# Optimization experiments

Measured on AMD Instinct MI355X. Metric: run time of the kernel, lower is better.

The kernel has to match this reference:

```python
import jax, jax.numpy as jnp
import numpy as np

N_NODES = 50000
IN_DIM = 256
LATENT = 128
HIDDEN = 2 * LATENT  # 256


def _xavier(key, fan_in, fan_out):
    # matches nn.init.xavier_uniform_ on a [out, in] weight; we store as [in, out]
    limit = float(np.sqrt(6.0 / (fan_in + fan_out)))
    return jax.random.uniform(key, (fan_in, fan_out), jnp.float32, -limit, limit)


def setup_inputs() -> dict:
    key = jax.random.key(0)
    ks = jax.random.split(key, 8)
    x = jax.random.normal(ks[0], (N_NODES, IN_DIM), jnp.float32)
    edge_index = jax.random.randint(ks[1], (2, 800000), 0, N_NODES, jnp.int64)
    W1 = _xavier(ks[2], IN_DIM, HIDDEN)
    b1 = jnp.zeros((HIDDEN,), jnp.float32)
    Wmu = _xavier(ks[3], HIDDEN, LATENT)
    bmu = jnp.zeros((LATENT,), jnp.float32)
    Wlv = _xavier(ks[4], HIDDEN, LATENT)
    blv = jnp.zeros((LATENT,), jnp.float32)
    return {"x": x, "edge_index": edge_index, "W1": W1, "b1": b1,
            "Wmu": Wmu, "bmu": bmu, "Wlv": Wlv, "blv": blv}


def _gcn_layer(x, W, b, src, dst):
    # PyG GCNConv: h = x @ W; add self loops; symmetric norm; scatter-add; + bias
    h = x @ W  # [N, out]
    ones = jnp.ones(src.shape[0], x.dtype)
    deg = jax.ops.segment_sum(ones, dst, num_segments=N_NODES) + 1.0  # +1 for self loop
    dinv = jax.lax.rsqrt(deg)  # deg >= 1 always
    norm = dinv[src] * dinv[dst]  # [E]
    agg = jax.ops.segment_sum(h[src] * norm[:, None], dst, num_segments=N_NODES)
    agg = agg + h * (dinv * dinv)[:, None]  # self-loop contribution, norm_ii = 1/deg_i
    return agg + b


def reference(x, edge_index, W1, b1, Wmu, bmu, Wlv, blv):
    src, dst = edge_index[0], edge_index[1]
    z = _gcn_layer(x, W1, b1, src, dst)
    z = jax.nn.relu(z)
    # dropout in eval mode == identity
    mu = _gcn_layer(z, Wmu, bmu, src, dst)
    logvar = _gcn_layer(z, Wlv, blv, src, dst)
    return (mu, logvar)
```

## Files before the change

kernel.cpp:

```cpp
#include <hip/hip_runtime.h>

#define N_NODES 50000
#define E_EDGES 800000
#define D 256
#define L 128
#define CAP 64

typedef __attribute__((ext_vector_type(8))) short bf16x8;
typedef __attribute__((ext_vector_type(4))) float f32x4;

__device__ __forceinline__ float bf2f(unsigned short u) {
    union { unsigned int i; float f; } v; v.i = ((unsigned int)u) << 16; return v.f;
}
__device__ __forceinline__ unsigned short f2bf(float f) {
    union { float f; unsigned int i; } v; v.f = f;
    unsigned int r = v.i + 0x7fffu + ((v.i >> 16) & 1u);
    return (unsigned short)(r >> 16);
}

__global__ __launch_bounds__(256) void setup_t(
    const float* __restrict__ W1, const float* __restrict__ Wmu,
    const float* __restrict__ Wlv, const float* __restrict__ bmu,
    const float* __restrict__ blv,
    unsigned short* __restrict__ W1h, unsigned short* __restrict__ W1l,
    unsigned short* __restrict__ Wch,
    float* __restrict__ bcat, int* __restrict__ cursor) {
    int b = blockIdx.x, t = threadIdx.x;
    if (b < 128) {
        __shared__ float tile[32][33];
        int m = b >> 6;
        int ti = b & 63;
        int k0 = (ti >> 3) * 32, n0 = (ti & 7) * 32;
        int rr = t >> 5, cc = t & 31;
#pragma unroll
        for (int p = 0; p < 4; ++p) {
            int kk = p * 8 + rr;
            int k = k0 + kk, n = n0 + cc;
            float w;
            if (m == 0) w = W1[k * 256 + n];
            else        w = (n < 128) ? Wmu[k * 128 + n] : Wlv[k * 128 + (n - 128)];
            tile[kk][cc] = w;
        }
        __syncthreads();
#pragma unroll
        for (int p = 0; p < 4; ++p) {
            int nn = p * 8 + rr;
            float w = tile[cc][nn];
            unsigned short h = f2bf(w);
            int n = n0 + nn, k = k0 + cc;
            if (m == 0) {
                W1h[n * 256 + k] = h;
                W1l[n * 256 + k] = f2bf(w - bf2f(h));
            } else {
                Wch[n * 256 + k] = h;
            }
        }
        if (b == 64) bcat[t] = (t < 128) ? bmu[t] : blv[t - 128];
    } else {
        int i = (b - 128) * 256 + t;
        if (i < N_NODES) cursor[i] = 0;
    }
}

__global__ __launch_bounds__(256, 2) void gemm1_fill(
    const float* __restrict__ A,
    const unsigned short* __restrict__ Bth, const unsigned short* __restrict__ Btl,
    unsigned short* __restrict__ Hout, int M,
    const int* __restrict__ src, const int* __restrict__ dst,
    int* __restrict__ cursor, unsigned short* __restrict__ bucket)
{
    __shared__ unsigned short Ash[128 * 32];
    __shared__ unsigned short Asl[128 * 32];
    __shared__ unsigned short Bsh[256 * 32];
    __shared__ unsigned short Bsl[256 * 32];
    const int bid = blockIdx.x;
    const int qb = bid / 9, rb = bid - qb * 9;
    const int t = threadIdx.x;

    if (rb != 0) {
        int e = (bid - qb - 1) * 256 + t;
        if (e < E_EDGES) {
            int d = dst[e];
            int pos = atomicAdd(&cursor[d], 1);
            if (pos < CAP) bucket[d * CAP + pos] = (unsigned short)src[e];
        }
        return;
    }

    const int lane = t & 63, wave = t >> 6;
    const int m_ = lane & 15, q = lane >> 4;
    const int wr = wave >> 1, wc = wave & 1;
    const int row0 = qb * 128;
    const int sr = t >> 2;
    const int sc = t & 3;

    f32x4 acc[4][8];
    const f32x4 zf = {0.f, 0.f, 0.f, 0.f};
#pragma unroll
    for (int rs = 0; rs < 4; ++rs)
#pragma unroll
        for (int nt = 0; nt < 8; ++nt) acc[rs][nt] = zf;

    for (int ks = 0; ks < 8; ++ks) {
        const int k0 = ks * 32;
        bf16x8 gbh[4], gbl[4];
#pragma unroll
        for (int i = 0; i < 4; ++i) {
            int n = sr + i * 64;
            gbh[i] = *(const bf16x8*)(Bth + n * 256 + k0 + sc * 8);
            gbl[i] = *(const bf16x8*)(Btl + n * 256 + k0 + sc * 8);
        }
        float4 ga0[2], ga1[2];
#pragma unroll
        for (int p = 0; p < 2; ++p) {
            int r = row0 + p * 64 + sr; if (r >= M) r = M - 1;
            const float* Xp = A + (size_t)r * 256 + k0 + sc * 8;
            ga0[p] = *(const float4*)Xp;
            ga1[p] = *(const float4*)(Xp + 4);
        }
        __syncthreads();
#pragma unroll
        for (int p = 0; p < 2; ++p) {
            int lr = p * 64 + sr;
            int cc = (sc ^ ((lr >> 1) & 3)) * 8;
            float af[8] = {ga0[p].x, ga0[p].y, ga0[p].z, ga0[p].w,
                           ga1[p].x, ga1[p].y, ga1[p].z, ga1[p].w};
            bf16x8 h, l;
#pragma unroll
            for (int j = 0; j < 8; ++j) {
                unsigned short hh = f2bf(af[j]);
                h[j] = (short)hh;
                l[j] = (short)f2bf(af[j] - bf2f(hh));
            }
            *(bf16x8*)&Ash[lr * 32 + cc] = h;
            *(bf16x8*)&Asl[lr * 32 + cc] = l;
        }
#pragma unroll
        for (int i = 0; i < 4; ++i) {
            int n = sr + i * 64;
            int cc = (sc ^ ((n >> 1) & 3)) * 8;
            *(bf16x8*)&Bsh[n * 32 + cc] = gbh[i];
            *(bf16x8*)&Bsl[n * 32 + cc] = gbl[i];
        }
        __syncthreads();
        bf16x8 ah[4], al[4];
#pragma unroll
        for (int rs = 0; rs < 4; ++rs) {
            int r = wr * 64 + rs * 16 + m_;
            int cc = (q ^ ((r >> 1) & 3)) * 8;
            ah[rs] = *(const bf16x8*)&Ash[r * 32 + cc];
            al[rs] = *(const bf16x8*)&Asl[r * 32 + cc];
        }
#pragma unroll
        for (int nt = 0; nt < 8; ++nt) {
            int n = wc * 128 + nt * 16 + m_;
            int cr = (q ^ ((n >> 1) & 3)) * 8;
            bf16x8 bh = *(const bf16x8*)&Bsh[n * 32 + cr];
            bf16x8 bl = *(const bf16x8*)&Bsl[n * 32 + cr];
#pragma unroll
            for (int rs = 0; rs < 4; ++rs) {
                acc[rs][nt] = __builtin_amdgcn_mfma_f32_16x16x32_bf16(ah[rs], bh, acc[rs][nt], 0, 0, 0);
                acc[rs][nt] = __builtin_amdgcn_mfma_f32_16x16x32_bf16(ah[rs], bl, acc[rs][nt], 0, 0, 0);
                acc[rs][nt] = __builtin_amdgcn_mfma_f32_16x16x32_bf16(al[rs], bh, acc[rs][nt], 0, 0, 0);
            }
        }
    }
#pragma unroll
    for (int rs = 0; rs < 4; ++rs) {
        int rbase = row0 + wr * 64 + rs * 16 + q * 4;
#pragma unroll
        for (int rr = 0; rr < 4; ++rr) {
            int grow = rbase + rr;
            if (grow >= M) continue;
#pragma unroll
            for (int nt = 0; nt < 8; ++nt) {
                int gcol = wc * 128 + nt * 16 + m_;
                Hout[(size_t)grow * 256 + gcol] = f2bf(acc[rs][nt][rr]);
            }
        }
    }
}

__global__ __launch_bounds__(256, 2) void gemm_bf16(
    const unsigned short* __restrict__ A,
    const unsigned short* __restrict__ Bth,
    unsigned short* __restrict__ Tout, int M)
{
    __shared__ unsigned short Ash[128 * 32];
    __shared__ unsigned short Bsh[256 * 32];
    const int t = threadIdx.x;
    const int lane = t & 63, wave = t >> 6;
    const int m_ = lane & 15, q = lane >> 4;
    const int wr = wave >> 1, wc = wave & 1;
    const int row0 = blockIdx.x * 128;
    const int sr = t >> 2;
    const int sc = t & 3;

    f32x4 acc[4][8];
    const f32x4 zf = {0.f, 0.f, 0.f, 0.f};
#pragma unroll
    for (int rs = 0; rs < 4; ++rs)
#pragma unroll
        for (int nt = 0; nt < 8; ++nt) acc[rs][nt] = zf;

    for (int ks = 0; ks < 8; ++ks) {
        const int k0 = ks * 32;
        bf16x8 gbh[4];
#pragma unroll
        for (int i = 0; i < 4; ++i) {
            int n = sr + i * 64;
            gbh[i] = *(const bf16x8*)(Bth + n * 256 + k0 + sc * 8);
        }
        bf16x8 gav[2];
#pragma unroll
        for (int p = 0; p < 2; ++p) {
            int r = row0 + p * 64 + sr; if (r >= M) r = M - 1;
            gav[p] = *(const bf16x8*)(A + (size_t)r * 256 + k0 + sc * 8);
        }
        __syncthreads();
#pragma unroll
        for (int p = 0; p < 2; ++p) {
            int lr = p * 64 + sr;
            int cc = (sc ^ ((lr >> 1) & 3)) * 8;
            *(bf16x8*)&Ash[lr * 32 + cc] = gav[p];
        }
#pragma unroll
        for (int i = 0; i < 4; ++i) {
            int n = sr + i * 64;
            int cc = (sc ^ ((n >> 1) & 3)) * 8;
            *(bf16x8*)&Bsh[n * 32 + cc] = gbh[i];
        }
        __syncthreads();
        bf16x8 ah[4];
#pragma unroll
        for (int rs = 0; rs < 4; ++rs) {
            int r = wr * 64 + rs * 16 + m_;
            int cc = (q ^ ((r >> 1) & 3)) * 8;
            ah[rs] = *(const bf16x8*)&Ash[r * 32 + cc];
        }
#pragma unroll
        for (int nt = 0; nt < 8; ++nt) {
            int n = wc * 128 + nt * 16 + m_;
            int cr = (q ^ ((n >> 1) & 3)) * 8;
            bf16x8 bh = *(const bf16x8*)&Bsh[n * 32 + cr];
#pragma unroll
            for (int rs = 0; rs < 4; ++rs) {
                acc[rs][nt] = __builtin_amdgcn_mfma_f32_16x16x32_bf16(ah[rs], bh, acc[rs][nt], 0, 0, 0);
            }
        }
    }
#pragma unroll
    for (int rs = 0; rs < 4; ++rs) {
        int rbase = row0 + wr * 64 + rs * 16 + q * 4;
#pragma unroll
        for (int rr = 0; rr < 4; ++rr) {
            int grow = rbase + rr;
            if (grow >= M) continue;
#pragma unroll
            for (int nt = 0; nt < 8; ++nt) {
                int gcol = wc * 128 + nt * 16 + m_;
                Tout[(size_t)grow * 256 + gcol] = f2bf(acc[rs][nt][rr]);
            }
        }
    }
}

__global__ __launch_bounds__(256) void gather_pre(
    const unsigned short* __restrict__ Hs,
    const unsigned short* __restrict__ bucket, const int* __restrict__ cnt_,
    const float* __restrict__ bias,
    unsigned short* __restrict__ OutZ,
    float* __restrict__ mu, float* __restrict__ lv, int mode, int node0)
{
    const int lane = threadIdx.x & 63;
    const int hl = lane & 31;
    const int bb = lane & 32;
    const int node = node0 + blockIdx.x * 8 + (threadIdx.x >> 5);
    const int col = hl * 8;
    int raw = cnt_[node];
    float dn = rsqrtf((float)raw + 1.0f);
    int cnt = raw > CAP ? CAP : raw;

    int   s0r = 0, s1r = 0;
    float w0r = 0.f, w1r = 0.f;
    if (hl < cnt) {
        s0r = (int)bucket[node * CAP + hl];
        w0r = rsqrtf((float)cnt_[s0r] + 1.0f) * dn;
    }
    if (hl + 32 < cnt) {
        s1r = (int)bucket[node * CAP + 32 + hl];
        w1r = rsqrtf((float)cnt_[s1r] + 1.0f) * dn;
    }

    float sl = dn * dn;
    bf16x8 hv = *(const bf16x8*)(Hs + (size_t)node * D + col);
    float a[8];
#pragma unroll
    for (int p = 0; p < 8; ++p) a[p] = bf2f((unsigned short)hv[p]) * sl;

    const int cnt0 = cnt < 32 ? cnt : 32;
    int j = 0;
    for (; j + 3 < cnt0; j += 4) {
        int t0 = __shfl(s0r, bb + j,     64), t1 = __shfl(s0r, bb + j + 1, 64);
        int t2 = __shfl(s0r, bb + j + 2, 64), t3 = __shfl(s0r, bb + j + 3, 64);
        float w0 = __shfl(w0r, bb + j,     64), w1 = __shfl(w0r, bb + j + 1, 64);
        float w2 = __shfl(w0r, bb + j + 2, 64), w3 = __shfl(w0r, bb + j + 3, 64);
        bf16x8 u0 = *(const bf16x8*)(Hs + (size_t)t0 * D + col);
        bf16x8 u1 = *(const bf16x8*)(Hs + (size_t)t1 * D + col);
        bf16x8 u2 = *(const bf16x8*)(Hs + (size_t)t2 * D + col);
        bf16x8 u3 = *(const bf16x8*)(Hs + (size_t)t3 * D + col);
#pragma unroll
        for (int p = 0; p < 8; ++p) a[p] = fmaf(bf2f((unsigned short)u0[p]), w0, a[p]);
#pragma unroll
        for (int p = 0; p < 8; ++p) a[p] = fmaf(bf2f((unsigned short)u1[p]), w1, a[p]);
#pragma unroll
        for (int p = 0; p < 8; ++p) a[p] = fmaf(bf2f((unsigned short)u2[p]), w2, a[p]);
#pragma unroll
        for (int p = 0; p < 8; ++p) a[p] = fmaf(bf2f((unsigned short)u3[p]), w3, a[p]);
    }
    for (; j < cnt0; ++j) {
        int   t0 = __shfl(s0r, bb + j, 64);
        float w0 = __shfl(w0r, bb + j, 64);
        bf16x8 u0 = *(const bf16x8*)(Hs + (size_t)t0 * D + col);
#pragma unroll
        for (int p = 0; p < 8; ++p) a[p] = fmaf(bf2f((unsigned short)u0[p]), w0, a[p]);
    }
    if (cnt > 32) {
        for (int j2 = 0; j2 < cnt - 32; ++j2) {
            int   t0 = __shfl(s1r, bb + j2, 64);
            float w0 = __shfl(w1r, bb + j2, 64);
            bf16x8 u0 = *(const bf16x8*)(Hs + (size_t)t0 * D + col);
#pragma unroll
            for (int p = 0; p < 8; ++p) a[p] = fmaf(bf2f((unsigned short)u0[p]), w0, a[p]);
        }
    }

    float4 b0 = *(const float4*)(bias + col);
    float4 b1 = *(const float4*)(bias + col + 4);
    float bf[8] = {b0.x, b0.y, b0.z, b0.w, b1.x, b1.y, b1.z, b1.w};
    if (mode == 0) {
        bf16x8 o;
#pragma unroll
        for (int p = 0; p < 8; ++p) o[p] = (short)f2bf(fmaxf(a[p] + bf[p], 0.f));
        *(bf16x8*)(OutZ + (size_t)node * D + col) = o;
    } else {
        float4 o0, o1;
        o0.x = a[0] + bf[0]; o0.y = a[1] + bf[1];
        o0.z = a[2] + bf[2]; o0.w = a[3] + bf[3];
        o1.x = a[4] + bf[4]; o1.y = a[5] + bf[5];
        o1.z = a[6] + bf[6]; o1.w = a[7] + bf[7];
        float* Op = (col < 128) ? (mu + (size_t)node * L + col)
                                : (lv + (size_t)node * L + (col - 128));
        *(float4*)Op = o0;
        *(float4*)(Op + 4) = o1;
    }
}

extern "C" void kernel_launch(void* const* d_in, const int* in_sizes, int n_in,
                              void* d_out, int out_size, void* d_ws, size_t ws_size,
                              hipStream_t stream) {
    const float* x   = (const float*)d_in[0];
    const int*   ei  = (const int*)d_in[1];
    const float* W1  = (const float*)d_in[2];
    const float* b1  = (const float*)d_in[3];
    const float* Wmu = (const float*)d_in[4];
    const float* bmu = (const float*)d_in[5];
    const float* Wlv = (const float*)d_in[6];
    const float* blv = (const float*)d_in[7];
    const int* src = ei;
    const int* dst = ei + E_EDGES;

    const size_t NF = (size_t)N_NODES * D;
    unsigned short* Hb = (unsigned short*)d_ws;
    unsigned short* Z  = Hb + NF;
    unsigned short* T  = Z + NF;
    unsigned short* W1h = T + NF;
    unsigned short* W1l = W1h + 65536;
    unsigned short* Wch = W1l + 65536;
    unsigned short* bucket = Wch + 65536;
    float* bcat = (float*)(bucket + (size_t)N_NODES * CAP);
    int* cursor = (int*)(bcat + 256);
    float* mu = (float*)d_out;
    float* lv = mu + (size_t)N_NODES * L;

    setup_t<<<128 + (N_NODES + 255) / 256, 256, 0, stream>>>(
        W1, Wmu, Wlv, bmu, blv, W1h, W1l, Wch, bcat, cursor);

    gemm1_fill<<<3516, 256, 0, stream>>>(x, W1h, W1l, Hb, N_NODES,
                                         src, dst, cursor, bucket);

    const int gemm_blocks = (N_NODES + 127) / 128;
    const int gat_blocks  = (N_NODES / 2) / 8;
    gather_pre<<<gat_blocks, 256, 0, stream>>>(Hb, bucket, cursor, b1,
                                               Z, nullptr, nullptr, 0, 0);
    gather_pre<<<gat_blocks, 256, 0, stream>>>(Hb, bucket, cursor, b1,
                                               Z, nullptr, nullptr, 0, N_NODES / 2);
    gemm_bf16<<<gemm_blocks, 256, 0, stream>>>(Z, Wch, T, N_NODES);
    gather_pre<<<gat_blocks, 256, 0, stream>>>(T, bucket, cursor, bcat,
                                               nullptr, mu, lv, 1, 0);
    gather_pre<<<gat_blocks, 256, 0, stream>>>(T, bucket, cursor, bcat,
                                               nullptr, mu, lv, 1, N_NODES / 2);
}
```

Baseline: 313.5 us.

## Build adjacency buckets with LDS-atomic partitioned fill and compaction pass

Replaces the global-atomic edge bucketing fused into the first GEMM with a separate two-stage build. Blocks own a range of destination nodes and an edge partition, count in LDS atomics, and write per-partition bucket segments. A compact kernel then merges them into the final bucket and degree arrays. This aims to remove contended global atomics, but every block rescans its whole edge partition (16x redundant reads of dst), it adds two launches, and it serialises the GEMM after the fill.

```diff
diff --git a/kernel.cpp b/kernel.cpp
--- a/kernel.cpp
+++ b/kernel.cpp
@@ -5,6 +5,12 @@
 #define D 256
 #define L 128
 #define CAP 64
+#define RB 16
+#define RNG 3125
+#define PARTS 4
+#define EPP 200000
+#define CAPSEG 24
+#define CAP96 (PARTS * CAPSEG)
 
 typedef __attribute__((ext_vector_type(8))) short bf16x8;
 typedef __attribute__((ext_vector_type(4))) float f32x4;
@@ -24,7 +30,7 @@
     const float* __restrict__ blv,
     unsigned short* __restrict__ W1h, unsigned short* __restrict__ W1l,
     unsigned short* __restrict__ Wch,
-    float* __restrict__ bcat, int* __restrict__ cursor) {
+    float* __restrict__ bcat, int* __restrict__ cnt4z) {
     int b = blockIdx.x, t = threadIdx.x;
     if (b < 128) {
         __shared__ float tile[32][33];
@@ -58,39 +64,77 @@
         if (b == 64) bcat[t] = (t < 128) ? bmu[t] : blv[t - 128];
     } else {
         int i = (b - 128) * 256 + t;
-        if (i < N_NODES) cursor[i] = 0;
-    }
-}
-
-__global__ __launch_bounds__(256, 2) void gemm1_fill(
+        if (i < (N_NODES * 4) / 2) cnt4z[i] = 0;
+    }
+}
+
+__global__ __launch_bounds__(256) void fill_lds(
+    const int* __restrict__ src, const int* __restrict__ dst,
+    unsigned short* __restrict__ cnt4,
+    unsigned short* __restrict__ bucket96)
+{
+    __shared__ int cnt[RNG];
+    const int t = threadIdx.x;
+    const int rb = blockIdx.x & (RB - 1);
+    const int p  = blockIdx.x >> 4;
+    const int base = rb * RNG;
+    for (int i = t; i < RNG; i += 256) cnt[i] = 0;
+    __syncthreads();
+    const int e0 = p * EPP;
+    for (int i = 0; i < (EPP + 255) / 256; ++i) {
+        int e = e0 + i * 256 + t;
+        if (e < e0 + EPP) {
+            int d = dst[e];
+            unsigned r = (unsigned)(d - base);
+            if (r < RNG) {
+                int slot = atomicAdd(&cnt[r], 1);
+                if (slot < CAPSEG)
+                    bucket96[(size_t)d * CAP96 + p * CAPSEG + slot] =
+                        (unsigned short)src[e];
+            }
+        }
+    }
+    __syncthreads();
+    for (int i = t; i < RNG; i += 256)
+        cnt4[(size_t)(base + i) * 4 + p] = (unsigned short)cnt[i];
+}
+
+__global__ __launch_bounds__(256) void compact(
+    const unsigned short* __restrict__ cnt4,
+    const unsigned short* __restrict__ bucket96,
+    unsigned short* __restrict__ bucket,
+    int* __restrict__ cursor)
+{
+    int n = blockIdx.x * 256 + threadIdx.x;
+    if (n >= N_NODES) return;
+    int c[4], deg = 0;
+#pragma unroll
+    for (int p = 0; p < 4; ++p) { c[p] = cnt4[(size_t)n * 4 + p]; deg += c[p]; }
+    cursor[n] = deg;
+    const unsigned short* in = bucket96 + (size_t)n * CAP96;
+    unsigned short* out = bucket + (size_t)n * CAP;
+    int k = 0;
+#pragma unroll
+    for (int p = 0; p < 4; ++p) {
+        int m = c[p] < CAPSEG ? c[p] : CAPSEG;
+        for (int j = 0; j < m && k < CAP; ++j) out[k++] = in[p * CAPSEG + j];
+    }
+}
+
+__global__ __launch_bounds__(256, 2) void gemm_mfma(
     const float* __restrict__ A,
     const unsigned short* __restrict__ Bth, const unsigned short* __restrict__ Btl,
-    unsigned short* __restrict__ Hout, int M,
-    const int* __restrict__ src, const int* __restrict__ dst,
-    int* __restrict__ cursor, unsigned short* __restrict__ bucket)
+    unsigned short* __restrict__ Hout, int M)
 {
     __shared__ unsigned short Ash[128 * 32];
     __shared__ unsigned short Asl[128 * 32];
     __shared__ unsigned short Bsh[256 * 32];
     __shared__ unsigned short Bsl[256 * 32];
-    const int bid = blockIdx.x;
-    const int qb = bid / 9, rb = bid - qb * 9;
     const int t = threadIdx.x;
-
-    if (rb != 0) {
-        int e = (bid - qb - 1) * 256 + t;
-        if (e < E_EDGES) {
-            int d = dst[e];
-            int pos = atomicAdd(&cursor[d], 1);
-            if (pos < CAP) bucket[d * CAP + pos] = (unsigned short)src[e];
-        }
-        return;
-    }
-
     const int lane = t & 63, wave = t >> 6;
     const int m_ = lane & 15, q = lane >> 4;
     const int wr = wave >> 1, wc = wave & 1;
-    const int row0 = qb * 128;
+    const int row0 = blockIdx.x * 128;
     const int sr = t >> 2;
     const int sc = t & 3;
 
@@ -377,20 +421,23 @@
     unsigned short* W1h = T + NF;
     unsigned short* W1l = W1h + 65536;
     unsigned short* Wch = W1l + 65536;
-    unsigned short* bucket = Wch + 65536;
-    float* bcat = (float*)(bucket + (size_t)N_NODES * CAP);
+    unsigned short* bucket   = Wch + 65536;
+    unsigned short* bucket96 = bucket + (size_t)N_NODES * CAP;
+    unsigned short* cnt4     = bucket96 + (size_t)N_NODES * CAP96;
+    float* bcat = (float*)(cnt4 + (size_t)N_NODES * 4);
     int* cursor = (int*)(bcat + 256);
     float* mu = (float*)d_out;
     float* lv = mu + (size_t)N_NODES * L;
 
-    setup_t<<<128 + (N_NODES + 255) / 256, 256, 0, stream>>>(
-        W1, Wmu, Wlv, bmu, blv, W1h, W1l, Wch, bcat, cursor);
-
-    gemm1_fill<<<3516, 256, 0, stream>>>(x, W1h, W1l, Hb, N_NODES,
-                                         src, dst, cursor, bucket);
+    setup_t<<<128 + ((N_NODES * 4) / 2 + 255) / 256, 256, 0, stream>>>(
+        W1, Wmu, Wlv, bmu, blv, W1h, W1l, Wch, bcat, (int*)cnt4);
+    fill_lds<<<RB * PARTS, 256, 0, stream>>>(src, dst, cnt4, bucket96);
+    compact<<<(N_NODES + 255) / 256, 256, 0, stream>>>(cnt4, bucket96,
+                                                       bucket, cursor);
 
     const int gemm_blocks = (N_NODES + 127) / 128;
     const int gat_blocks  = (N_NODES / 2) / 8;
+    gemm_mfma<<<gemm_blocks, 256, 0, stream>>>(x, W1h, W1l, Hb, N_NODES);
     gather_pre<<<gat_blocks, 256, 0, stream>>>(Hb, bucket, cursor, b1,
                                                Z, nullptr, nullptr, 0, 0);
     gather_pre<<<gat_blocks, 256, 0, stream>>>(Hb, bucket, cursor, b1,
```

Result: slower. 774.3 us (+147.0%).

## Fuse layer-1 gather with second GEMM, dropping Z round-trip and split launches

Applied to the files above, without the earlier changes.

The first-layer aggregation now writes its ReLU output for 8 nodes into shared memory, and the same block runs the 8x256 by 256x256 MFMA product against the concatenated mu/logvar weights. This removes the Z intermediate buffer write and read and the separate GEMM launch. The half-split gather launches are merged into single full-size launches. The cost is that each block reloads the whole 256x256 weight matrix from global or L2 with no LDS reuse. Only 8 of the 16 MFMA rows carry real data, so half the matrix-core work is wasted.

```diff
diff --git a/kernel.cpp b/kernel.cpp
--- a/kernel.cpp
+++ b/kernel.cpp
@@ -5,6 +5,7 @@
 #define D 256
 #define L 128
 #define CAP 64
+#define ZLD 264
 
 typedef __attribute__((ext_vector_type(8))) short bf16x8;
 typedef __attribute__((ext_vector_type(4))) float f32x4;
@@ -181,101 +182,21 @@
     }
 }
 
-__global__ __launch_bounds__(256, 2) void gemm_bf16(
-    const unsigned short* __restrict__ A,
-    const unsigned short* __restrict__ Bth,
-    unsigned short* __restrict__ Tout, int M)
-{
-    __shared__ unsigned short Ash[128 * 32];
-    __shared__ unsigned short Bsh[256 * 32];
-    const int t = threadIdx.x;
-    const int lane = t & 63, wave = t >> 6;
-    const int m_ = lane & 15, q = lane >> 4;
-    const int wr = wave >> 1, wc = wave & 1;
-    const int row0 = blockIdx.x * 128;
-    const int sr = t >> 2;
-    const int sc = t & 3;
-
-    f32x4 acc[4][8];
-    const f32x4 zf = {0.f, 0.f, 0.f, 0.f};
-#pragma unroll
-    for (int rs = 0; rs < 4; ++rs)
-#pragma unroll
-        for (int nt = 0; nt < 8; ++nt) acc[rs][nt] = zf;
-
-    for (int ks = 0; ks < 8; ++ks) {
-        const int k0 = ks * 32;
-        bf16x8 gbh[4];
-#pragma unroll
-        for (int i = 0; i < 4; ++i) {
-            int n = sr + i * 64;
-            gbh[i] = *(const bf16x8*)(Bth + n * 256 + k0 + sc * 8);
-        }
-        bf16x8 gav[2];
-#pragma unroll
-        for (int p = 0; p < 2; ++p) {
-            int r = row0 + p * 64 + sr; if (r >= M) r = M - 1;
-            gav[p] = *(const bf16x8*)(A + (size_t)r * 256 + k0 + sc * 8);
-        }
-        __syncthreads();
-#pragma unroll
-        for (int p = 0; p < 2; ++p) {
-            int lr = p * 64 + sr;
-            int cc = (sc ^ ((lr >> 1) & 3)) * 8;
-            *(bf16x8*)&Ash[lr * 32 + cc] = gav[p];
-        }
-#pragma unroll
-        for (int i = 0; i < 4; ++i) {
-            int n = sr + i * 64;
-            int cc = (sc ^ ((n >> 1) & 3)) * 8;
-            *(bf16x8*)&Bsh[n * 32 + cc] = gbh[i];
-        }
-        __syncthreads();
-        bf16x8 ah[4];
-#pragma unroll
-        for (int rs = 0; rs < 4; ++rs) {
-            int r = wr * 64 + rs * 16 + m_;
-            int cc = (q ^ ((r >> 1) & 3)) * 8;
-            ah[rs] = *(const bf16x8*)&Ash[r * 32 + cc];
-        }
-#pragma unroll
-        for (int nt = 0; nt < 8; ++nt) {
-            int n = wc * 128 + nt * 16 + m_;
-            int cr = (q ^ ((n >> 1) & 3)) * 8;
-            bf16x8 bh = *(const bf16x8*)&Bsh[n * 32 + cr];
-#pragma unroll
-            for (int rs = 0; rs < 4; ++rs) {
-                acc[rs][nt] = __builtin_amdgcn_mfma_f32_16x16x32_bf16(ah[rs], bh, acc[rs][nt], 0, 0, 0);
-            }
-        }
-    }
-#pragma unroll
-    for (int rs = 0; rs < 4; ++rs) {
-        int rbase = row0 + wr * 64 + rs * 16 + q * 4;
-#pragma unroll
-        for (int rr = 0; rr < 4; ++rr) {
-            int grow = rbase + rr;
-            if (grow >= M) continue;
-#pragma unroll
-            for (int nt = 0; nt < 8; ++nt) {
-                int gcol = wc * 128 + nt * 16 + m_;
-                Tout[(size_t)grow * 256 + gcol] = f2bf(acc[rs][nt][rr]);
-            }
-        }
-    }
-}
-
-__global__ __launch_bounds__(256) void gather_pre(
+__global__ __launch_bounds__(256) void gather_gemm(
     const unsigned short* __restrict__ Hs,
     const unsigned short* __restrict__ bucket, const int* __restrict__ cnt_,
     const float* __restrict__ bias,
-    unsigned short* __restrict__ OutZ,
-    float* __restrict__ mu, float* __restrict__ lv, int mode, int node0)
+    const unsigned short* __restrict__ Wch,
+    unsigned short* __restrict__ Tout)
 {
-    const int lane = threadIdx.x & 63;
+    __shared__ unsigned short Zs[8 * ZLD];
+    const int t = threadIdx.x;
+    const int lane = t & 63;
     const int hl = lane & 31;
     const int bb = lane & 32;
-    const int node = node0 + blockIdx.x * 8 + (threadIdx.x >> 5);
+    const int lrow = t >> 5;
+    const int nb0 = blockIdx.x * 8;
+    const int node = nb0 + lrow;
     const int col = hl * 8;
     int raw = cnt_[node];
     float dn = rsqrtf((float)raw + 1.0f);
@@ -335,25 +256,126 @@
         }
     }
 
+    {
+        float4 b0 = *(const float4*)(bias + col);
+        float4 b1v = *(const float4*)(bias + col + 4);
+        float bf[8] = {b0.x, b0.y, b0.z, b0.w, b1v.x, b1v.y, b1v.z, b1v.w};
+        bf16x8 o;
+#pragma unroll
+        for (int p = 0; p < 8; ++p) o[p] = (short)f2bf(fmaxf(a[p] + bf[p], 0.f));
+        *(bf16x8*)&Zs[lrow * ZLD + col] = o;
+    }
+    __syncthreads();
+
+    const int m_ = lane & 15, q = lane >> 4;
+    const int wv = t >> 6;
+    f32x4 tacc[4];
+    const f32x4 zf = {0.f, 0.f, 0.f, 0.f};
+#pragma unroll
+    for (int nt = 0; nt < 4; ++nt) tacc[nt] = zf;
+#pragma unroll
+    for (int ks = 0; ks < 8; ++ks) {
+        bf16x8 ah = *(const bf16x8*)&Zs[(m_ & 7) * ZLD + ks * 32 + q * 8];
+#pragma unroll
+        for (int nt = 0; nt < 4; ++nt) {
+            int n = wv * 64 + nt * 16 + m_;
+            bf16x8 bh = *(const bf16x8*)(Wch + n * 256 + ks * 32 + q * 8);
+            tacc[nt] = __builtin_amdgcn_mfma_f32_16x16x32_bf16(ah, bh, tacc[nt], 0, 0, 0);
+        }
+    }
+    if (q < 2) {
+#pragma unroll
+        for (int r = 0; r < 4; ++r) {
+            int row = q * 4 + r;
+            unsigned short* Tp = Tout + (size_t)(nb0 + row) * 256;
+#pragma unroll
+            for (int nt = 0; nt < 4; ++nt) {
+                int gcol = wv * 64 + nt * 16 + m_;
+                Tp[gcol] = f2bf(tacc[nt][r]);
+            }
+        }
+    }
+}
+
+__global__ __launch_bounds__(256) void gather_out(
+    const unsigned short* __restrict__ Hs,
+    const unsigned short* __restrict__ bucket, const int* __restrict__ cnt_,
+    const float* __restrict__ bias,
+    float* __restrict__ mu, float* __restrict__ lv)
+{
+    const int lane = threadIdx.x & 63;
+    const int hl = lane & 31;
+    const int bb = lane & 32;
+    const int node = blockIdx.x * 8 + (threadIdx.x >> 5);
+    const int col = hl * 8;
+    int raw = cnt_[node];
+    float dn = rsqrtf((float)raw + 1.0f);
+    int cnt = raw > CAP ? CAP : raw;
+
+    int   s0r = 0, s1r = 0;
+    float w0r = 0.f, w1r = 0.f;
+    if (hl < cnt) {
+        s0r = (int)bucket[node * CAP + hl];
+        w0r = rsqrtf((float)cnt_[s0r] + 1.0f) * dn;
+    }
+    if (hl + 32 < cnt) {
+        s1r = (int)bucket[node * CAP + 32 + hl];
+        w1r = rsqrtf((float)cnt_[s1r] + 1.0f) * dn;
+    }
+
+    float sl = dn * dn;
+    bf16x8 hv = *(const bf16x8*)(Hs + (size_t)node * D + col);
+    float a[8];
+#pragma unroll
+    for (int p = 0; p < 8; ++p) a[p] = bf2f((unsigned short)hv[p]) * sl;
+
+    const int cnt0 = cnt < 32 ? cnt : 32;
+    int j = 0;
+    for (; j + 3 < cnt0; j += 4) {
+        int t0 = __shfl(s0r, bb + j,     64), t1 = __shfl(s0r, bb + j + 1, 64);
+        int t2 = __shfl(s0r, bb + j + 2, 64), t3 = __shfl(s0r, bb + j + 3, 64);
+        float w0 = __shfl(w0r, bb + j,     64), w1 = __shfl(w0r, bb + j + 1, 64);
+        float w2 = __shfl(w0r, bb + j + 2, 64), w3 = __shfl(w0r, bb + j + 3, 64);
+        bf16x8 u0 = *(const bf16x8*)(Hs + (size_t)t0 * D + col);
+        bf16x8 u1 = *(const bf16x8*)(Hs + (size_t)t1 * D + col);
+        bf16x8 u2 = *(const bf16x8*)(Hs + (size_t)t2 * D + col);
+        bf16x8 u3 = *(const bf16x8*)(Hs + (size_t)t3 * D + col);
+#pragma unroll
+        for (int p = 0; p < 8; ++p) a[p] = fmaf(bf2f((unsigned short)u0[p]), w0, a[p]);
+#pragma unroll
+        for (int p = 0; p < 8; ++p) a[p] = fmaf(bf2f((unsigned short)u1[p]), w1, a[p]);
+#pragma unroll
+        for (int p = 0; p < 8; ++p) a[p] = fmaf(bf2f((unsigned short)u2[p]), w2, a[p]);
+#pragma unroll
+        for (int p = 0; p < 8; ++p) a[p] = fmaf(bf2f((unsigned short)u3[p]), w3, a[p]);
+    }
+    for (; j < cnt0; ++j) {
+        int   t0 = __shfl(s0r, bb + j, 64);
+        float w0 = __shfl(w0r, bb + j, 64);
+        bf16x8 u0 = *(const bf16x8*)(Hs + (size_t)t0 * D + col);
+#pragma unroll
+        for (int p = 0; p < 8; ++p) a[p] = fmaf(bf2f((unsigned short)u0[p]), w0, a[p]);
+    }
+    if (cnt > 32) {
+        for (int j2 = 0; j2 < cnt - 32; ++j2) {
+            int   t0 = __shfl(s1r, bb + j2, 64);
+            float w0 = __shfl(w1r, bb + j2, 64);
+            bf16x8 u0 = *(const bf16x8*)(Hs + (size_t)t0 * D + col);
+#pragma unroll
+            for (int p = 0; p < 8; ++p) a[p] = fmaf(bf2f((unsigned short)u0[p]), w0, a[p]);
+        }
+    }
+
     float4 b0 = *(const float4*)(bias + col);
     float4 b1 = *(const float4*)(bias + col + 4);
-    float bf[8] = {b0.x, b0.y, b0.z, b0.w, b1.x, b1.y, b1.z, b1.w};
-    if (mode == 0) {
-        bf16x8 o;
-#pragma unroll
-        for (int p = 0; p < 8; ++p) o[p] = (short)f2bf(fmaxf(a[p] + bf[p], 0.f));
-        *(bf16x8*)(OutZ + (size_t)node * D + col) = o;
-    } else {
-        float4 o0, o1;
-        o0.x = a[0] + bf[0]; o0.y = a[1] + bf[1];
-        o0.z = a[2] + bf[2]; o0.w = a[3] + bf[3];
-        o1.x = a[4] + bf[4]; o1.y = a[5] + bf[5];
-        o1.z = a[6] + bf[6]; o1.w = a[7] + bf[7];
-        float* Op = (col < 128) ? (mu + (size_t)node * L + col)
-                                : (lv + (size_t)node * L + (col - 128));
-        *(float4*)Op = o0;
-        *(float4*)(Op + 4) = o1;
-    }
+    float o0x = a[0] + b0.x, o0y = a[1] + b0.y, o0z = a[2] + b0.z, o0w = a[3] + b0.w;
+    float o1x = a[4] + b1.x, o1y = a[5] + b1.y, o1z = a[6] + b1.z, o1w = a[7] + b1.w;
+    float4 o0 = {o0x, o0y, o0z, o0w};
+    float4 o1 = {o1x, o1y, o1z, o1w};
+    float* Op = (col < 128) ? (mu + (size_t)node * L + col)
+                            : (lv + (size_t)node * L + (col - 128));
+    *(float4*)Op = o0;
+    *(float4*)(Op + 4) = o1;
 }
 
 extern "C" void kernel_launch(void* const* d_in, const int* in_sizes, int n_in,
@@ -372,8 +394,7 @@
 
     const size_t NF = (size_t)N_NODES * D;
     unsigned short* Hb = (unsigned short*)d_ws;
-    unsigned short* Z  = Hb + NF;
-    unsigned short* T  = Z + NF;
+    unsigned short* T  = Hb + NF;
     unsigned short* W1h = T + NF;
     unsigned short* W1l = W1h + 65536;
     unsigned short* Wch = W1l + 65536;
@@ -389,15 +410,9 @@
     gemm1_fill<<<3516, 256, 0, stream>>>(x, W1h, W1l, Hb, N_NODES,
                                          src, dst, cursor, bucket);
 
-    const int gemm_blocks = (N_NODES + 127) / 128;
-    const int gat_blocks  = (N_NODES / 2) / 8;
-    gather_pre<<<gat_blocks, 256, 0, stream>>>(Hb, bucket, cursor, b1,
-                                               Z, nullptr, nullptr, 0, 0);
-    gather_pre<<<gat_blocks, 256, 0, stream>>>(Hb, bucket, cursor, b1,
-                                               Z, nullptr, nullptr, 0, N_NODES / 2);
-    gemm_bf16<<<gemm_blocks, 256, 0, stream>>>(Z, Wch, T, N_NODES);
-    gather_pre<<<gat_blocks, 256, 0, stream>>>(T, bucket, cursor, bcat,
-                                               nullptr, mu, lv, 1, 0);
-    gather_pre<<<gat_blocks, 256, 0, stream>>>(T, bucket, cursor, bcat,
-                                               nullptr, mu, lv, 1, N_NODES / 2);
-}
+    const int gat_blocks = N_NODES / 8;
+    gather_gemm<<<gat_blocks, 256, 0, stream>>>(Hb, bucket, cursor, b1,
+                                                Wch, T);
+    gather_out<<<gat_blocks, 256, 0, stream>>>(T, bucket, cursor, bcat,
+                                               mu, lv);
+}
```

Result: slower. 349.7 us (+11.6%).
